# Kernel optimization log

Hardware: AMD Instinct MI355X
Metric: run time of the kernel (lower is better)

## Reference

```python
import jax, jax.numpy as jnp
import numpy as np

B, S, D, H = 8, 1024, 1024, 16
DH = D // H


def setup_inputs() -> dict:
    key = jax.random.key(0)
    ks = jax.random.split(key, 8)
    en = jax.random.normal(ks[0], (B, S, D), dtype=jnp.float32)
    fr = jax.random.normal(ks[1], (B, S, D), dtype=jnp.float32)
    l_en = jax.random.randint(ks[2], (B,), 1, S + 1)
    l_fr = jax.random.randint(ks[3], (B,), 1, S + 1)
    # nn.Linear-style params (weight stored [out, in])
    lim_q = 1.0 / np.sqrt(D)
    W_Q_w = jax.random.uniform(ks[4], (D, D), minval=-lim_q, maxval=lim_q, dtype=jnp.float32)
    W_Q_b = jax.random.uniform(ks[5], (D,), minval=-lim_q, maxval=lim_q, dtype=jnp.float32)
    W_KV_w = jax.random.uniform(ks[6], (2 * D, D), minval=-lim_q, maxval=lim_q, dtype=jnp.float32)
    W_KV_b = jax.random.uniform(ks[7], (2 * D,), minval=-lim_q, maxval=lim_q, dtype=jnp.float32)
    return {"en": en, "fr": fr, "l_en": l_en, "l_fr": l_fr,
            "W_Q_w": W_Q_w, "W_Q_b": W_Q_b, "W_KV_w": W_KV_w, "W_KV_b": W_KV_b}


def reference(en, fr, l_en, l_fr, W_Q_w, W_Q_b, W_KV_w, W_KV_b):
    # q from decoder (fr), k/v from encoder (en)
    q = (fr @ W_Q_w.T + W_Q_b).reshape(B, S, H, DH).transpose(0, 2, 1, 3)  # [B,H,S,DH]
    kv = (en @ W_KV_w.T + W_KV_b).reshape(B, S, 2, H, DH).transpose(2, 0, 3, 1, 4)
    k, v = kv[0], kv[1]  # [B,H,S,DH]

    # NOTE: original scales by sqrt(embedding_dim), not sqrt(head_dim)
    attn = jnp.einsum('bhqd,bhkd->bhqk', q, k) / jnp.sqrt(jnp.float32(D))

    pos = jnp.arange(S)
    mask_en = (pos[None, :] < l_en[:, None])  # [B,S] key mask
    mask_fr = (pos[None, :] < l_fr[:, None])  # [B,S] query mask
    mask = (mask_fr[:, :, None] & mask_en[:, None, :])[:, None, :, :]  # [B,1,Sq,Sk]

    attn = jnp.where(mask, attn, -jnp.inf)
    attn = jax.nn.softmax(attn, axis=-1)
    attn = jnp.nan_to_num(attn)  # fully-masked rows -> 0 (matches torch nan_to_num)

    out = jnp.einsum('bhqk,bhkd->bhqd', attn, v)  # [B,H,S,DH]
    return out.transpose(0, 2, 1, 3).reshape(B, S, D)
```

## Files before the change

### kernel.cpp

```cpp
#include <hip/hip_runtime.h>
#include <hip/hip_bf16.h>
#include <stdint.h>

typedef __bf16 bf16_t;
typedef bf16_t bf16x8 __attribute__((ext_vector_type(8)));
typedef float f32x4 __attribute__((ext_vector_type(4)));
typedef unsigned short ushortx8 __attribute__((ext_vector_type(8)));

__device__ __forceinline__ uint16_t f2bf(float f) {
  uint32_t u = __float_as_uint(f);
  uint32_t r = u + 0x7FFFu + ((u >> 16) & 1u);
  return (uint16_t)(r >> 16);
}

__device__ __forceinline__ int read_len(const int* __restrict__ p, int b) {
  bool is64 = (p[1] == 0) | (p[3] == 0) | (p[5] == 0) | (p[7] == 0);
  return is64 ? p[2 * b] : p[b];
}

#define GLDS16(gp, lp)                                                   \
  __builtin_amdgcn_global_load_lds(                                      \
      (const __attribute__((address_space(1))) uint32_t*)(gp),           \
      (__attribute__((address_space(3))) uint32_t*)(lp), 16, 0, 0)

__global__ void cvt4_kernel(const float* __restrict__ s0, uint16_t* __restrict__ d0, int n0,
                            const float* __restrict__ s1, uint16_t* __restrict__ d1, int n1,
                            const float* __restrict__ s2, uint16_t* __restrict__ d2, int n2,
                            const float* __restrict__ s3, uint16_t* __restrict__ d3, int n3,
                            const int* __restrict__ msk0, const int* __restrict__ msk1) {
  int e = (blockIdx.x * blockDim.x + threadIdx.x) * 8;
  const float* s;
  uint16_t* d;
  const int* msk = nullptr;
  if (e < n0) { s = s0 + e; d = d0 + e; msk = msk0; }
  else if ((e -= n0) < n1) { s = s1 + e; d = d1 + e; msk = msk1; }
  else if ((e -= n1) < n2) { s = s2 + e; d = d2 + e; }
  else if ((e -= n2) < n3) { s = s3 + e; d = d3 + e; }
  else return;
  if (msk) {
    int row = (e >> 10) & 1023, b = e >> 20;
    int need = (read_len(msk, b) + 127) & ~127;
    if (row >= need) return;
  }
  const float4 v0 = *reinterpret_cast<const float4*>(s);
  const float4 v1 = *reinterpret_cast<const float4*>(s + 4);
  ushortx8 o;
  o[0] = f2bf(v0.x); o[1] = f2bf(v0.y); o[2] = f2bf(v0.z); o[3] = f2bf(v0.w);
  o[4] = f2bf(v1.x); o[5] = f2bf(v1.y); o[6] = f2bf(v1.z); o[7] = f2bf(v1.w);
  *reinterpret_cast<ushortx8*>(d) = o;
}

__global__ __launch_bounds__(512) void gemm_fast(
    const uint16_t* __restrict__ frB, const uint16_t* __restrict__ enB,
    const uint16_t* __restrict__ wq, const uint16_t* __restrict__ wkv,
    const float* __restrict__ bq, const float* __restrict__ bkv,
    const int* __restrict__ l_en_p, const int* __restrict__ l_fr_p,
    uint16_t* __restrict__ Qb,
    uint16_t* __restrict__ Kb,
    uint16_t* __restrict__ Vb) {
  __shared__ __attribute__((aligned(16))) uint16_t As[3][128 * 64];
  __shared__ __attribute__((aligned(16))) uint16_t Bs[2][128 * 64];
  const int t = threadIdx.x;
  const int lane = t & 63;
  const int w = t >> 6;
  const int wm = w >> 2, wn = w & 3;
  const int l15 = lane & 15, lg = lane >> 4;

  const int orig = blockIdx.x;
  const int xcd = orig & 7;
  const int slot = orig >> 3;
  const bool isQ = slot < 64;
  int b, bn;
  if (isQ) { b = slot >> 3; bn = (slot & 7) * 128; }
  else { int s2 = slot - 64; b = s2 >> 4; bn = (s2 & 15) * 128; }
  const int i = (xcd - b) & 7;
  const int bm = b * 1024 + i * 128;

  const int need = isQ ? read_len(l_fr_p, b) : read_len(l_en_p, b);
  if (i * 128 >= need) return;

  const uint16_t* Bw = isQ ? wq : wkv;
  const float* bias = isQ ? bq : bkv;
  const float scale = isQ ? 0.03125f : 1.0f;
  const uint16_t* Ab = isQ ? frB : enB;

  f32x4 acc[4][2];
#pragma unroll
  for (int ii = 0; ii < 4; ++ii)
#pragma unroll
    for (int j = 0; j < 2; ++j) acc[ii][j] = (f32x4){0.f, 0.f, 0.f, 0.f};

  auto stageB = [&](int buf, int kt) {
#pragma unroll
    for (int ii = 0; ii < 2; ++ii) {
      int g = t + 512 * ii;
      int L = g ^ ((g >> 3) & 7);
      int row = L >> 3, k8 = L & 7;
      GLDS16(Bw + (size_t)(bn + row) * 1024 + kt + k8 * 8, &Bs[buf][g * 8]);
    }
  };
  auto stageA = [&](int buf, int kt) {
#pragma unroll
    for (int ii = 0; ii < 2; ++ii) {
      int g = t + 512 * ii;
      int L = g ^ ((g >> 3) & 7);
      int row = L >> 3, k8 = L & 7;
      GLDS16(Ab + (size_t)(bm + row) * 1024 + kt + k8 * 8, &As[buf][g * 8]);
    }
  };
  auto computeAB = [&](int bufA, int bufB) {
#pragma unroll
    for (int ks = 0; ks < 2; ++ks) {
      const int kb = ks * 64 + lg * 16;
      bf16x8 af[4], bf[2];
#pragma unroll
      for (int mf = 0; mf < 4; ++mf) {
        int row = wm * 64 + mf * 16 + l15;
        int byte = (row * 128 + kb) ^ ((row & 7) << 4);
        af[mf] = *reinterpret_cast<const bf16x8*>(
            reinterpret_cast<const char*>(As[bufA]) + byte);
      }
#pragma unroll
      for (int nf = 0; nf < 2; ++nf) {
        int row = wn * 32 + nf * 16 + l15;
        int byte = (row * 128 + kb) ^ ((row & 7) << 4);
        bf[nf] = *reinterpret_cast<const bf16x8*>(
            reinterpret_cast<const char*>(Bs[bufB]) + byte);
      }
#pragma unroll
      for (int mf = 0; mf < 4; ++mf)
#pragma unroll
        for (int nf = 0; nf < 2; ++nf)
          acc[mf][nf] = __builtin_amdgcn_mfma_f32_16x16x32_bf16(
              af[mf], bf[nf], acc[mf][nf], 0, 0, 0);
    }
  };

  stageA(0, 0);
  stageB(0, 0);
  stageA(1, 64);
  asm volatile("s_waitcnt vmcnt(2)" ::: "memory");
  __builtin_amdgcn_s_barrier();
  __builtin_amdgcn_sched_barrier(0);
  int aC = 0, bC = 0;
  for (int tt = 0; tt < 16; ++tt) {
    if (tt + 1 < 16) stageB(bC ^ 1, (tt + 1) * 64);
    if (tt + 2 < 16) stageA(aC >= 1 ? aC - 1 : aC + 2, (tt + 2) * 64);
    computeAB(aC, bC);
    if (tt < 15) {
      if (tt < 14) asm volatile("s_waitcnt vmcnt(2)" ::: "memory");
      else         asm volatile("s_waitcnt vmcnt(0)" ::: "memory");
      __builtin_amdgcn_s_barrier();
      __builtin_amdgcn_sched_barrier(0);
    }
    aC = (aC == 2) ? 0 : aC + 1;
    bC ^= 1;
  }

#pragma unroll
  for (int mf = 0; mf < 4; ++mf) {
#pragma unroll
    for (int nf = 0; nf < 2; ++nf) {
      int n = bn + wn * 32 + nf * 16 + l15;
      float bv = bias[n];
#pragma unroll
      for (int r = 0; r < 4; ++r) {
        int m = bm + wm * 64 + mf * 16 + lg * 4 + r;
        float v = (acc[mf][nf][r] + bv) * scale;
        uint16_t o = f2bf(v);
        int bb = m >> 10, s = m & 1023;
        if (isQ) {
          int h = n >> 6, d = n & 63;
          Qb[((((bb * 16 + h) << 10) | s) << 6) | d] = o;
        } else if (n < 1024) {
          int h = n >> 6, d = n & 63;
          Kb[((((bb * 16 + h) << 10) | s) << 6) | d] = o;
        } else {
          int n2 = n - 1024;
          int h = n2 >> 6, d = n2 & 63;
          Vb[((((bb * 16 + h) << 6) | d) << 10) | s] = o;
        }
      }
    }
  }
}

__global__ __launch_bounds__(256) void gemm_fb(
    const float* __restrict__ frF, const float* __restrict__ enF,
    const uint16_t* __restrict__ wq, const uint16_t* __restrict__ wkv,
    const float* __restrict__ bq, const float* __restrict__ bkv,
    const int* __restrict__ l_en_p, const int* __restrict__ l_fr_p,
    uint16_t* __restrict__ Qb, uint16_t* __restrict__ Kb,
    uint16_t* __restrict__ Vb) {
  __shared__ __attribute__((aligned(16))) uint16_t As[2][128 * 64];
  __shared__ __attribute__((aligned(16))) uint16_t Bs[2][128 * 64];
  const int t = threadIdx.x;
  const int lane = t & 63;
  const int w = t >> 6;
  const int wm = w >> 1, wn = w & 1;
  const int l15 = lane & 15, lg = lane >> 4;

  const int orig = blockIdx.x;
  const int xcd = orig & 7;
  const int slot = orig >> 3;
  const bool isQ = slot < 64;
  int b, bn;
  if (isQ) { b = slot >> 3; bn = (slot & 7) * 128; }
  else { int s2 = slot - 64; b = s2 >> 4; bn = (s2 & 15) * 128; }
  const int i = (xcd - b) & 7;
  const int bm = b * 1024 + i * 128;

  const int need = isQ ? read_len(l_fr_p, b) : read_len(l_en_p, b);
  if (i * 128 >= need) return;

  const uint16_t* Bw = isQ ? wq : wkv;
  const float* bias = isQ ? bq : bkv;
  const float scale = isQ ? 0.03125f : 1.0f;
  const float* Af = isQ ? frF : enF;

  f32x4 acc[4][4];
#pragma unroll
  for (int ii = 0; ii < 4; ++ii)
#pragma unroll
    for (int j = 0; j < 4; ++j) acc[ii][j] = (f32x4){0.f, 0.f, 0.f, 0.f};

  float4 ar0[4], ar1[4];

  auto stageB = [&](int buf, int kt) {
#pragma unroll
    for (int ii = 0; ii < 4; ++ii) {
      int g = t + 256 * ii;
      int L = g ^ ((g >> 3) & 7);
      int row = L >> 3, k8 = L & 7;
      GLDS16(Bw + (size_t)(bn + row) * 1024 + kt + k8 * 8, &Bs[buf][g * 8]);
    }
  };
  auto loadA_f32 = [&](int kt) {
#pragma unroll
    for (int ii = 0; ii < 4; ++ii) {
      int L = t + 256 * ii;
      int row = L >> 3, k8 = L & 7;
      const float* src = Af + (size_t)(bm + row) * 1024 + kt + k8 * 8;
      ar0[ii] = *reinterpret_cast<const float4*>(src);
      ar1[ii] = *reinterpret_cast<const float4*>(src + 4);
    }
  };
  auto writeA = [&](int buf) {
#pragma unroll
    for (int ii = 0; ii < 4; ++ii) {
      int L = t + 256 * ii;
      int row = L >> 3, k8 = L & 7;
      ushortx8 o;
      o[0] = f2bf(ar0[ii].x); o[1] = f2bf(ar0[ii].y);
      o[2] = f2bf(ar0[ii].z); o[3] = f2bf(ar0[ii].w);
      o[4] = f2bf(ar1[ii].x); o[5] = f2bf(ar1[ii].y);
      o[6] = f2bf(ar1[ii].z); o[7] = f2bf(ar1[ii].w);
      int byte = (row * 128 + k8 * 16) ^ ((row & 7) << 4);
      *reinterpret_cast<ushortx8*>(reinterpret_cast<char*>(As[buf]) + byte) = o;
    }
  };
  auto compute = [&](int buf) {
#pragma unroll
    for (int ks = 0; ks < 2; ++ks) {
      const int kb = ks * 64 + lg * 16;
      bf16x8 af[4], bf[4];
#pragma unroll
      for (int mf = 0; mf < 4; ++mf) {
        int row = wm * 64 + mf * 16 + l15;
        int byte = (row * 128 + kb) ^ ((row & 7) << 4);
        af[mf] = *reinterpret_cast<const bf16x8*>(
            reinterpret_cast<const char*>(As[buf]) + byte);
      }
#pragma unroll
      for (int nf = 0; nf < 4; ++nf) {
        int row = wn * 64 + nf * 16 + l15;
        int byte = (row * 128 + kb) ^ ((row & 7) << 4);
        bf[nf] = *reinterpret_cast<const bf16x8*>(
            reinterpret_cast<const char*>(Bs[buf]) + byte);
      }
#pragma unroll
      for (int mf = 0; mf < 4; ++mf)
#pragma unroll
        for (int nf = 0; nf < 4; ++nf)
          acc[mf][nf] = __builtin_amdgcn_mfma_f32_16x16x32_bf16(
              af[mf], bf[nf], acc[mf][nf], 0, 0, 0);
    }
  };
  loadA_f32(0);
  stageB(0, 0);
  writeA(0);
  __syncthreads();
#pragma unroll 2
  for (int tt = 0; tt < 16; ++tt) {
    const int cur = tt & 1;
    const int ktn = (tt + 1) * 64;
    if (tt < 15) { stageB(cur ^ 1, ktn); loadA_f32(ktn); }
    compute(cur);
    if (tt < 15) writeA(cur ^ 1);
    __syncthreads();
  }

#pragma unroll
  for (int mf = 0; mf < 4; ++mf) {
#pragma unroll
    for (int nf = 0; nf < 4; ++nf) {
      int n = bn + wn * 64 + nf * 16 + l15;
      float bv = bias[n];
#pragma unroll
      for (int r = 0; r < 4; ++r) {
        int m = bm + wm * 64 + mf * 16 + lg * 4 + r;
        float v = (acc[mf][nf][r] + bv) * scale;
        uint16_t o = f2bf(v);
        int bb = m >> 10, s = m & 1023;
        if (isQ) {
          int h = n >> 6, d = n & 63;
          Qb[((((bb * 16 + h) << 10) | s) << 6) | d] = o;
        } else if (n < 1024) {
          int h = n >> 6, d = n & 63;
          Kb[((((bb * 16 + h) << 10) | s) << 6) | d] = o;
        } else {
          int n2 = n - 1024;
          int h = n2 >> 6, d = n2 & 63;
          Vb[((((bb * 16 + h) << 6) | d) << 10) | s] = o;
        }
      }
    }
  }
}

__global__ __launch_bounds__(512) void attn_kernel(
    const uint16_t* __restrict__ Qb,
    const uint16_t* __restrict__ Kb,
    const uint16_t* __restrict__ Vt,
    const int* __restrict__ l_en_p, const int* __restrict__ l_fr_p,
    float* __restrict__ out) {
  __shared__ __attribute__((aligned(16))) uint16_t Ks[3][64 * 64];
  __shared__ __attribute__((aligned(16))) uint16_t Vs[3][64 * 64];
  __shared__ __attribute__((aligned(16))) bf16_t Ps[8][16][72];
  const int t = threadIdx.x;
  const int lane = t & 63, w = t >> 6;
  const int l15 = lane & 15, lg = lane >> 4;
  const int orig = blockIdx.x;
  const int xcd = orig & 7;
  const int slot = orig >> 3;
  const int b = slot >> 4;
  const int rest = slot & 15;
  const int h = xcd + 8 * (rest >> 3);
  const int q0 = (rest & 7) << 7;
  const int bh = b * 16 + h;
  const int len_en = read_len(l_en_p, b);
  const int len_fr = read_len(l_fr_p, b);

  if (q0 >= len_fr) {
    for (int i = t; i < 128 * 64; i += 512) {
      int rr = i >> 6, cc = i & 63;
      out[(size_t)(b * 1024 + q0 + rr) * 1024 + h * 64 + cc] = 0.f;
    }
    return;
  }

  const uint16_t* qbase =
      Qb + ((size_t)bh * 1024 + q0 + w * 16 + l15) * 64 + lg * 8;
  const bf16x8 aq0 = *reinterpret_cast<const bf16x8*>(qbase);
  const bf16x8 aq1 = *reinterpret_cast<const bf16x8*>(qbase + 32);

  float mrow[4], lrow[4];
  f32x4 oacc[4];
#pragma unroll
  for (int r = 0; r < 4; ++r) { mrow[r] = -1e30f; lrow[r] = 0.f; }
#pragma unroll
  for (int df = 0; df < 4; ++df) oacc[df] = (f32x4){0.f, 0.f, 0.f, 0.f};

  auto stage = [&](int buf, int j0) {
    int g = t;
    int L = g ^ ((g >> 3) & 7);
    int row = L >> 3, k8 = L & 7;
    GLDS16(Kb + ((size_t)bh * 1024 + j0 + row) * 64 + k8 * 8, &Ks[buf][g * 8]);
    GLDS16(Vt + ((size_t)bh * 64 + row) * 1024 + j0 + k8 * 8, &Vs[buf][g * 8]);
  };

  const int ntiles = (len_en + 63) >> 6;
  stage(0, 0);
  if (ntiles > 1) {
    stage(1, 64);
    asm volatile("s_waitcnt vmcnt(2)" ::: "memory");
  } else {
    asm volatile("s_waitcnt vmcnt(0)" ::: "memory");
  }
  __builtin_amdgcn_s_barrier();
  __builtin_amdgcn_sched_barrier(0);

  int cur = 0;
  for (int tt = 0; tt < ntiles; ++tt) {
    const int j0 = tt * 64;
    if (tt + 2 < ntiles) stage(cur >= 1 ? cur - 1 : 2, (tt + 2) * 64);

    f32x4 sc[4];
#pragma unroll
    for (int nf = 0; nf < 4; ++nf) sc[nf] = (f32x4){0.f, 0.f, 0.f, 0.f};
    __builtin_amdgcn_s_setprio(1);
#pragma unroll
    for (int ks = 0; ks < 2; ++ks) {
      const bf16x8 aq = ks ? aq1 : aq0;
      const int kb = ks * 64 + lg * 16;
#pragma unroll
      for (int nf = 0; nf < 4; ++nf) {
        int row = nf * 16 + l15;
        int byte = (row * 128 + kb) ^ ((row & 7) << 4);
        bf16x8 bk = *reinterpret_cast<const bf16x8*>(
            reinterpret_cast<const char*>(Ks[cur]) + byte);
        sc[nf] = __builtin_amdgcn_mfma_f32_16x16x32_bf16(aq, bk, sc[nf], 0, 0, 0);
      }
    }
    __builtin_amdgcn_s_setprio(0);
#pragma unroll
    for (int nf = 0; nf < 4; ++nf) {
      int col = j0 + nf * 16 + l15;
      if (col >= len_en) sc[nf] = (f32x4){-1e30f, -1e30f, -1e30f, -1e30f};
    }
    float tm[4];
#pragma unroll
    for (int r = 0; r < 4; ++r)
      tm[r] = fmaxf(fmaxf(sc[0][r], sc[1][r]), fmaxf(sc[2][r], sc[3][r]));
#pragma unroll
    for (int off = 1; off < 16; off <<= 1)
#pragma unroll
      for (int r = 0; r < 4; ++r) tm[r] = fmaxf(tm[r], __shfl_xor(tm[r], off));

    bool small = (tm[0] <= mrow[0] + 8.f) && (tm[1] <= mrow[1] + 8.f) &&
                 (tm[2] <= mrow[2] + 8.f) && (tm[3] <= mrow[3] + 8.f);
    if (!__all(small)) {
      float fac[4];
#pragma unroll
      for (int r = 0; r < 4; ++r) {
        float mn = fmaxf(mrow[r], tm[r]);
        fac[r] = __expf(mrow[r] - mn);
        mrow[r] = mn;
      }
#pragma unroll
      for (int r = 0; r < 4; ++r) lrow[r] *= fac[r];
#pragma unroll
      for (int df = 0; df < 4; ++df)
#pragma unroll
        for (int r = 0; r < 4; ++r) oacc[df][r] *= fac[r];
    }
    float ps[4] = {0.f, 0.f, 0.f, 0.f};
#pragma unroll
    for (int nf = 0; nf < 4; ++nf)
#pragma unroll
      for (int r = 0; r < 4; ++r) {
        float p = __expf(sc[nf][r] - mrow[r]);
        ps[r] += p;
        Ps[w][lg * 4 + r][nf * 16 + l15] = (bf16_t)p;
      }
#pragma unroll
    for (int off = 1; off < 16; off <<= 1)
#pragma unroll
      for (int r = 0; r < 4; ++r) ps[r] += __shfl_xor(ps[r], off);
#pragma unroll
    for (int r = 0; r < 4; ++r) lrow[r] += ps[r];

    __builtin_amdgcn_s_setprio(1);
#pragma unroll
    for (int ks = 0; ks < 2; ++ks) {
      const bf16x8 pa = *reinterpret_cast<const bf16x8*>(
          &Ps[w][l15][0] + ks * 32 + lg * 8);
#pragma unroll
      for (int df = 0; df < 4; ++df) {
        int row = df * 16 + l15;
        int byte = (row * 128 + ks * 64 + lg * 16) ^ ((row & 7) << 4);
        bf16x8 bv = *reinterpret_cast<const bf16x8*>(
            reinterpret_cast<const char*>(Vs[cur]) + byte);
        oacc[df] = __builtin_amdgcn_mfma_f32_16x16x32_bf16(pa, bv, oacc[df], 0, 0, 0);
      }
    }
    __builtin_amdgcn_s_setprio(0);

    if (tt + 1 < ntiles) {
      if (tt + 2 < ntiles) asm volatile("s_waitcnt vmcnt(2)" ::: "memory");
      else                 asm volatile("s_waitcnt vmcnt(0)" ::: "memory");
      __builtin_amdgcn_s_barrier();
      __builtin_amdgcn_sched_barrier(0);
    }
    cur = (cur == 2) ? 0 : cur + 1;
  }

#pragma unroll
  for (int df = 0; df < 4; ++df)
#pragma unroll
    for (int r = 0; r < 4; ++r) {
      int q = q0 + w * 16 + lg * 4 + r;
      float inv = (q < len_fr && lrow[r] > 0.f) ? 1.0f / lrow[r] : 0.f;
      out[(size_t)(b * 1024 + q) * 1024 + h * 64 + df * 16 + l15] =
          oacc[df][r] * inv;
    }
}

extern "C" void kernel_launch(void* const* d_in, const int* in_sizes, int n_in,
                              void* d_out, int out_size, void* d_ws,
                              size_t ws_size, hipStream_t stream) {
  const float* en = (const float*)d_in[0];
  const float* fr = (const float*)d_in[1];
  const int* l_en = (const int*)d_in[2];
  const int* l_fr = (const int*)d_in[3];
  const float* wq = (const float*)d_in[4];
  const float* bq = (const float*)d_in[5];
  const float* wkv = (const float*)d_in[6];
  const float* bkv = (const float*)d_in[7];
  float* out = (float*)d_out;

  char* ws = (char*)d_ws;
  uint16_t* wq_bf = (uint16_t*)(ws);
  uint16_t* wkv_bf = (uint16_t*)(ws + 2097152);
  uint16_t* Qbuf = (uint16_t*)(ws + 6291456);
  uint16_t* Kbuf = (uint16_t*)(ws + 23068672);
  uint16_t* Vtbuf = (uint16_t*)(ws + 39845888);
  uint16_t* fr_bf = (uint16_t*)(ws + 56623104);
  uint16_t* en_bf = (uint16_t*)(ws + 73400320);
  const bool pre = ws_size >= 90177536ull;

  if (pre) {
    cvt4_kernel<<<9728, 256, 0, stream>>>(fr, fr_bf, 8388608,
                                          en, en_bf, 8388608,
                                          wq, wq_bf, 1048576,
                                          wkv, wkv_bf, 2097152,
                                          l_fr, l_en);
    gemm_fast<<<1536, 512, 0, stream>>>(fr_bf, en_bf, wq_bf, wkv_bf, bq, bkv,
                                        l_en, l_fr, Qbuf, Kbuf, Vtbuf);
  } else {
    cvt4_kernel<<<1536, 256, 0, stream>>>(wq, wq_bf, 1048576,
                                          wkv, wkv_bf, 2097152,
                                          nullptr, nullptr, 0,
                                          nullptr, nullptr, 0,
                                          nullptr, nullptr);
    gemm_fb<<<1536, 256, 0, stream>>>(fr, en, wq_bf, wkv_bf, bq, bkv,
                                      l_en, l_fr, Qbuf, Kbuf, Vtbuf);
  }

  attn_kernel<<<1024, 512, 0, stream>>>(Qbuf, Kbuf, Vtbuf, l_en, l_fr, out);
}
```

Measured before the change: 108.2 us.

## Use persistent blocks with per-XCD atomic work counters in GEMM and attention

Converts gemm_fast and attn_kernel into persistent kernels launched with 512 blocks. Each block repeatedly pulls a slot index from a per-XCD global atomic counter, and the counters are reset at the start of the conversion kernel. The goal is to balance work when masked tiles exit early with uneven cost, and to avoid the launch and tail cost of many short blocks. In exchange it adds atomic and barrier overhead per work item, and it depends on the conversion kernel always running first to reset the counters.

```diff
diff --git a/kernel.cpp b/kernel.cpp
--- a/kernel.cpp
+++ b/kernel.cpp
@@ -6,6 +6,9 @@
 typedef bf16_t bf16x8 __attribute__((ext_vector_type(8)));
 typedef float f32x4 __attribute__((ext_vector_type(4)));
 typedef unsigned short ushortx8 __attribute__((ext_vector_type(8)));
+
+__device__ int g_qctr[8];
+__device__ int g_actr[8];
 
 __device__ __forceinline__ uint16_t f2bf(float f) {
   uint32_t u = __float_as_uint(f);
@@ -28,6 +31,10 @@
                             const float* __restrict__ s2, uint16_t* __restrict__ d2, int n2,
                             const float* __restrict__ s3, uint16_t* __restrict__ d3, int n3,
                             const int* __restrict__ msk0, const int* __restrict__ msk1) {
+  if (blockIdx.x == 0 && threadIdx.x < 16) {
+    if (threadIdx.x < 8) g_qctr[threadIdx.x] = 0;
+    else g_actr[threadIdx.x - 8] = 0;
+  }
   int e = (blockIdx.x * blockDim.x + threadIdx.x) * 8;
   const float* s;
   uint16_t* d;
@@ -60,10 +67,150 @@
     uint16_t* __restrict__ Vb) {
   __shared__ __attribute__((aligned(16))) uint16_t As[3][128 * 64];
   __shared__ __attribute__((aligned(16))) uint16_t Bs[2][128 * 64];
+  __shared__ int slot_sh;
   const int t = threadIdx.x;
   const int lane = t & 63;
   const int w = t >> 6;
   const int wm = w >> 2, wn = w & 3;
+  const int l15 = lane & 15, lg = lane >> 4;
+  const int xcd = blockIdx.x & 7;
+
+  for (;;) {
+    if (t == 0) slot_sh = atomicAdd(&g_qctr[xcd], 1);
+    __syncthreads();
+    const int slot = slot_sh;
+    __syncthreads();
+    if (slot >= 192) break;
+
+    const bool isQ = slot < 64;
+    int b, bn;
+    if (isQ) { b = slot >> 3; bn = (slot & 7) * 128; }
+    else { int s2 = slot - 64; b = s2 >> 4; bn = (s2 & 15) * 128; }
+    const int i = (xcd - b) & 7;
+    const int bm = b * 1024 + i * 128;
+    const int need = isQ ? read_len(l_fr_p, b) : read_len(l_en_p, b);
+    if (i * 128 >= need) continue;
+
+    const uint16_t* Bw = isQ ? wq : wkv;
+    const float* bias = isQ ? bq : bkv;
+    const float scale = isQ ? 0.03125f : 1.0f;
+    const uint16_t* Ab = isQ ? frB : enB;
+
+    f32x4 acc[4][2];
+#pragma unroll
+    for (int ii = 0; ii < 4; ++ii)
+#pragma unroll
+      for (int j = 0; j < 2; ++j) acc[ii][j] = (f32x4){0.f, 0.f, 0.f, 0.f};
+
+    auto stageB = [&](int buf, int kt) {
+#pragma unroll
+      for (int ii = 0; ii < 2; ++ii) {
+        int g = t + 512 * ii;
+        int L = g ^ ((g >> 3) & 7);
+        int row = L >> 3, k8 = L & 7;
+        GLDS16(Bw + (size_t)(bn + row) * 1024 + kt + k8 * 8, &Bs[buf][g * 8]);
+      }
+    };
+    auto stageA = [&](int buf, int kt) {
+#pragma unroll
+      for (int ii = 0; ii < 2; ++ii) {
+        int g = t + 512 * ii;
+        int L = g ^ ((g >> 3) & 7);
+        int row = L >> 3, k8 = L & 7;
+        GLDS16(Ab + (size_t)(bm + row) * 1024 + kt + k8 * 8, &As[buf][g * 8]);
+      }
+    };
+    auto computeAB = [&](int bufA, int bufB) {
+#pragma unroll
+      for (int ks = 0; ks < 2; ++ks) {
+        const int kb = ks * 64 + lg * 16;
+        bf16x8 af[4], bf[2];
+#pragma unroll
+        for (int mf = 0; mf < 4; ++mf) {
+          int row = wm * 64 + mf * 16 + l15;
+          int byte = (row * 128 + kb) ^ ((row & 7) << 4);
+          af[mf] = *reinterpret_cast<const bf16x8*>(
+              reinterpret_cast<const char*>(As[bufA]) + byte);
+        }
+#pragma unroll
+        for (int nf = 0; nf < 2; ++nf) {
+          int row = wn * 32 + nf * 16 + l15;
+          int byte = (row * 128 + kb) ^ ((row & 7) << 4);
+          bf[nf] = *reinterpret_cast<const bf16x8*>(
+              reinterpret_cast<const char*>(Bs[bufB]) + byte);
+        }
+#pragma unroll
+        for (int mf = 0; mf < 4; ++mf)
+#pragma unroll
+          for (int nf = 0; nf < 2; ++nf)
+            acc[mf][nf] = __builtin_amdgcn_mfma_f32_16x16x32_bf16(
+                af[mf], bf[nf], acc[mf][nf], 0, 0, 0);
+      }
+    };
+
+    stageA(0, 0);
+    stageB(0, 0);
+    stageA(1, 64);
+    asm volatile("s_waitcnt vmcnt(2)" ::: "memory");
+    __builtin_amdgcn_s_barrier();
+    __builtin_amdgcn_sched_barrier(0);
+    int aC = 0, bC = 0;
+    for (int tt = 0; tt < 16; ++tt) {
+      if (tt + 1 < 16) stageB(bC ^ 1, (tt + 1) * 64);
+      if (tt + 2 < 16) stageA(aC >= 1 ? aC - 1 : aC + 2, (tt + 2) * 64);
+      computeAB(aC, bC);
+      if (tt < 15) {
+        if (tt < 14) asm volatile("s_waitcnt vmcnt(2)" ::: "memory");
+        else         asm volatile("s_waitcnt vmcnt(0)" ::: "memory");
+        __builtin_amdgcn_s_barrier();
+        __builtin_amdgcn_sched_barrier(0);
+      }
+      aC = (aC == 2) ? 0 : aC + 1;
+      bC ^= 1;
+    }
+
+#pragma unroll
+    for (int mf = 0; mf < 4; ++mf) {
+#pragma unroll
+      for (int nf = 0; nf < 2; ++nf) {
+        int n = bn + wn * 32 + nf * 16 + l15;
+        float bv = bias[n];
+#pragma unroll
+        for (int r = 0; r < 4; ++r) {
+          int m = bm + wm * 64 + mf * 16 + lg * 4 + r;
+          float v = (acc[mf][nf][r] + bv) * scale;
+          uint16_t o = f2bf(v);
+          int bb = m >> 10, s = m & 1023;
+          if (isQ) {
+            int h = n >> 6, d = n & 63;
+            Qb[((((bb * 16 + h) << 10) | s) << 6) | d] = o;
+          } else if (n < 1024) {
+            int h = n >> 6, d = n & 63;
+            Kb[((((bb * 16 + h) << 10) | s) << 6) | d] = o;
+          } else {
+            int n2 = n - 1024;
+            int h = n2 >> 6, d = n2 & 63;
+            Vb[((((bb * 16 + h) << 6) | d) << 10) | s] = o;
+          }
+        }
+      }
+    }
+  }
+}
+
+__global__ __launch_bounds__(256) void gemm_fb(
+    const float* __restrict__ frF, const float* __restrict__ enF,
+    const uint16_t* __restrict__ wq, const uint16_t* __restrict__ wkv,
+    const float* __restrict__ bq, const float* __restrict__ bkv,
+    const int* __restrict__ l_en_p, const int* __restrict__ l_fr_p,
+    uint16_t* __restrict__ Qb, uint16_t* __restrict__ Kb,
+    uint16_t* __restrict__ Vb) {
+  __shared__ __attribute__((aligned(16))) uint16_t As[2][128 * 64];
+  __shared__ __attribute__((aligned(16))) uint16_t Bs[2][128 * 64];
+  const int t = threadIdx.x;
+  const int lane = t & 63;
+  const int w = t >> 6;
+  const int wm = w >> 1, wn = w & 1;
   const int l15 = lane & 15, lg = lane >> 4;
 
   const int orig = blockIdx.x;
@@ -82,86 +229,95 @@
   const uint16_t* Bw = isQ ? wq : wkv;
   const float* bias = isQ ? bq : bkv;
   const float scale = isQ ? 0.03125f : 1.0f;
-  const uint16_t* Ab = isQ ? frB : enB;
-
-  f32x4 acc[4][2];
+  const float* Af = isQ ? frF : enF;
+
+  f32x4 acc[4][4];
 #pragma unroll
   for (int ii = 0; ii < 4; ++ii)
 #pragma unroll
-    for (int j = 0; j < 2; ++j) acc[ii][j] = (f32x4){0.f, 0.f, 0.f, 0.f};
+    for (int j = 0; j < 4; ++j) acc[ii][j] = (f32x4){0.f, 0.f, 0.f, 0.f};
+
+  float4 ar0[4], ar1[4];
 
   auto stageB = [&](int buf, int kt) {
 #pragma unroll
-    for (int ii = 0; ii < 2; ++ii) {
-      int g = t + 512 * ii;
+    for (int ii = 0; ii < 4; ++ii) {
+      int g = t + 256 * ii;
       int L = g ^ ((g >> 3) & 7);
       int row = L >> 3, k8 = L & 7;
       GLDS16(Bw + (size_t)(bn + row) * 1024 + kt + k8 * 8, &Bs[buf][g * 8]);
     }
   };
-  auto stageA = [&](int buf, int kt) {
-#pragma unroll
-    for (int ii = 0; ii < 2; ++ii) {
-      int g = t + 512 * ii;
-      int L = g ^ ((g >> 3) & 7);
+  auto loadA_f32 = [&](int kt) {
+#pragma unroll
+    for (int ii = 0; ii < 4; ++ii) {
+      int L = t + 256 * ii;
       int row = L >> 3, k8 = L & 7;
-      GLDS16(Ab + (size_t)(bm + row) * 1024 + kt + k8 * 8, &As[buf][g * 8]);
+      const float* src = Af + (size_t)(bm + row) * 1024 + kt + k8 * 8;
+      ar0[ii] = *reinterpret_cast<const float4*>(src);
+      ar1[ii] = *reinterpret_cast<const float4*>(src + 4);
     }
   };
-  auto computeAB = [&](int bufA, int bufB) {
+  auto writeA = [&](int buf) {
+#pragma unroll
+    for (int ii = 0; ii < 4; ++ii) {
+      int L = t + 256 * ii;
+      int row = L >> 3, k8 = L & 7;
+      ushortx8 o;
+      o[0] = f2bf(ar0[ii].x); o[1] = f2bf(ar0[ii].y);
+      o[2] = f2bf(ar0[ii].z); o[3] = f2bf(ar0[ii].w);
+      o[4] = f2bf(ar1[ii].x); o[5] = f2bf(ar1[ii].y);
+      o[6] = f2bf(ar1[ii].z); o[7] = f2bf(ar1[ii].w);
+      int byte = (row * 128 + k8 * 16) ^ ((row & 7) << 4);
+      *reinterpret_cast<ushortx8*>(reinterpret_cast<char*>(As[buf]) + byte) = o;
+    }
+  };
+  auto compute = [&](int buf) {
 #pragma unroll
     for (int ks = 0; ks < 2; ++ks) {
       const int kb = ks * 64 + lg * 16;
-      bf16x8 af[4], bf[2];
+      bf16x8 af[4], bf[4];
 #pragma unroll
       for (int mf = 0; mf < 4; ++mf) {
         int row = wm * 64 + mf * 16 + l15;
         int byte = (row * 128 + kb) ^ ((row & 7) << 4);
         af[mf] = *reinterpret_cast<const bf16x8*>(
-            reinterpret_cast<const char*>(As[bufA]) + byte);
-      }
-#pragma unroll
-      for (int nf = 0; nf < 2; ++nf) {
-        int row = wn * 32 + nf * 16 + l15;
+            reinterpret_cast<const char*>(As[buf]) + byte);
+      }
+#pragma unroll
+      for (int nf = 0; nf < 4; ++nf) {
+        int row = wn * 64 + nf * 16 + l15;
         int byte = (row * 128 + kb) ^ ((row & 7) << 4);
         bf[nf] = *reinterpret_cast<const bf16x8*>(
-            reinterpret_cast<const char*>(Bs[bufB]) + byte);
+            reinterpret_cast<const char*>(Bs[buf]) + byte);
       }
 #pragma unroll
       for (int mf = 0; mf < 4; ++mf)
 #pragma unroll
-        for (int nf = 0; nf < 2; ++nf)
+        for (int nf = 0; nf < 4; ++nf)
           acc[mf][nf] = __builtin_amdgcn_mfma_f32_16x16x32_bf16(
               af[mf], bf[nf], acc[mf][nf], 0, 0, 0);
     }
   };
-
-  stageA(0, 0);
+  loadA_f32(0);
   stageB(0, 0);
-  stageA(1, 64);
-  asm volatile("s_waitcnt vmcnt(2)" ::: "memory");
-  __builtin_amdgcn_s_barrier();
-  __builtin_amdgcn_sched_barrier(0);
-  int aC = 0, bC = 0;
+  writeA(0);
+  __syncthreads();
+#pragma unroll 2
   for (int tt = 0; tt < 16; ++tt) {
-    if (tt + 1 < 16) stageB(bC ^ 1, (tt + 1) * 64);
-    if (tt + 2 < 16) stageA(aC >= 1 ? aC - 1 : aC + 2, (tt + 2) * 64);
-    computeAB(aC, bC);
-    if (tt < 15) {
-      if (tt < 14) asm volatile("s_waitcnt vmcnt(2)" ::: "memory");
-      else         asm volatile("s_waitcnt vmcnt(0)" ::: "memory");
-      __builtin_amdgcn_s_barrier();
-      __builtin_amdgcn_sched_barrier(0);
-    }
-    aC = (aC == 2) ? 0 : aC + 1;
-    bC ^= 1;
+    const int cur = tt & 1;
+    const int ktn = (tt + 1) * 64;
+    if (tt < 15) { stageB(cur ^ 1, ktn); loadA_f32(ktn); }
+    compute(cur);
+    if (tt < 15) writeA(cur ^ 1);
+    __syncthreads();
   }
 
 #pragma unroll
   for (int mf = 0; mf < 4; ++mf) {
 #pragma unroll
-    for (int nf = 0; nf < 2; ++nf) {
-      int n = bn + wn * 32 + nf * 16 + l15;
+    for (int nf = 0; nf < 4; ++nf) {
+      int n = bn + wn * 64 + nf * 16 + l15;
       float bv = bias[n];
 #pragma unroll
       for (int r = 0; r < 4; ++r) {
@@ -185,149 +341,6 @@
   }
 }
 
-__global__ __launch_bounds__(256) void gemm_fb(
-    const float* __restrict__ frF, const float* __restrict__ enF,
-    const uint16_t* __restrict__ wq, const uint16_t* __restrict__ wkv,
-    const float* __restrict__ bq, const float* __restrict__ bkv,
-    const int* __restrict__ l_en_p, const int* __restrict__ l_fr_p,
-    uint16_t* __restrict__ Qb, uint16_t* __restrict__ Kb,
-    uint16_t* __restrict__ Vb) {
-  __shared__ __attribute__((aligned(16))) uint16_t As[2][128 * 64];
-  __shared__ __attribute__((aligned(16))) uint16_t Bs[2][128 * 64];
-  const int t = threadIdx.x;
-  const int lane = t & 63;
-  const int w = t >> 6;
-  const int wm = w >> 1, wn = w & 1;
-  const int l15 = lane & 15, lg = lane >> 4;
-
-  const int orig = blockIdx.x;
-  const int xcd = orig & 7;
-  const int slot = orig >> 3;
-  const bool isQ = slot < 64;
-  int b, bn;
-  if (isQ) { b = slot >> 3; bn = (slot & 7) * 128; }
-  else { int s2 = slot - 64; b = s2 >> 4; bn = (s2 & 15) * 128; }
-  const int i = (xcd - b) & 7;
-  const int bm = b * 1024 + i * 128;
-
-  const int need = isQ ? read_len(l_fr_p, b) : read_len(l_en_p, b);
-  if (i * 128 >= need) return;
-
-  const uint16_t* Bw = isQ ? wq : wkv;
-  const float* bias = isQ ? bq : bkv;
-  const float scale = isQ ? 0.03125f : 1.0f;
-  const float* Af = isQ ? frF : enF;
-
-  f32x4 acc[4][4];
-#pragma unroll
-  for (int ii = 0; ii < 4; ++ii)
-#pragma unroll
-    for (int j = 0; j < 4; ++j) acc[ii][j] = (f32x4){0.f, 0.f, 0.f, 0.f};
-
-  float4 ar0[4], ar1[4];
-
-  auto stageB = [&](int buf, int kt) {
-#pragma unroll
-    for (int ii = 0; ii < 4; ++ii) {
-      int g = t + 256 * ii;
-      int L = g ^ ((g >> 3) & 7);
-      int row = L >> 3, k8 = L & 7;
-      GLDS16(Bw + (size_t)(bn + row) * 1024 + kt + k8 * 8, &Bs[buf][g * 8]);
-    }
-  };
-  auto loadA_f32 = [&](int kt) {
-#pragma unroll
-    for (int ii = 0; ii < 4; ++ii) {
-      int L = t + 256 * ii;
-      int row = L >> 3, k8 = L & 7;
-      const float* src = Af + (size_t)(bm + row) * 1024 + kt + k8 * 8;
-      ar0[ii] = *reinterpret_cast<const float4*>(src);
-      ar1[ii] = *reinterpret_cast<const float4*>(src + 4);
-    }
-  };
-  auto writeA = [&](int buf) {
-#pragma unroll
-    for (int ii = 0; ii < 4; ++ii) {
-      int L = t + 256 * ii;
-      int row = L >> 3, k8 = L & 7;
-      ushortx8 o;
-      o[0] = f2bf(ar0[ii].x); o[1] = f2bf(ar0[ii].y);
-      o[2] = f2bf(ar0[ii].z); o[3] = f2bf(ar0[ii].w);
-      o[4] = f2bf(ar1[ii].x); o[5] = f2bf(ar1[ii].y);
-      o[6] = f2bf(ar1[ii].z); o[7] = f2bf(ar1[ii].w);
-      int byte = (row * 128 + k8 * 16) ^ ((row & 7) << 4);
-      *reinterpret_cast<ushortx8*>(reinterpret_cast<char*>(As[buf]) + byte) = o;
-    }
-  };
-  auto compute = [&](int buf) {
-#pragma unroll
-    for (int ks = 0; ks < 2; ++ks) {
-      const int kb = ks * 64 + lg * 16;
-      bf16x8 af[4], bf[4];
-#pragma unroll
-      for (int mf = 0; mf < 4; ++mf) {
-        int row = wm * 64 + mf * 16 + l15;
-        int byte = (row * 128 + kb) ^ ((row & 7) << 4);
-        af[mf] = *reinterpret_cast<const bf16x8*>(
-            reinterpret_cast<const char*>(As[buf]) + byte);
-      }
-#pragma unroll
-      for (int nf = 0; nf < 4; ++nf) {
-        int row = wn * 64 + nf * 16 + l15;
-        int byte = (row * 128 + kb) ^ ((row & 7) << 4);
-        bf[nf] = *reinterpret_cast<const bf16x8*>(
-            reinterpret_cast<const char*>(Bs[buf]) + byte);
-      }
-#pragma unroll
-      for (int mf = 0; mf < 4; ++mf)
-#pragma unroll
-        for (int nf = 0; nf < 4; ++nf)
-          acc[mf][nf] = __builtin_amdgcn_mfma_f32_16x16x32_bf16(
-              af[mf], bf[nf], acc[mf][nf], 0, 0, 0);
-    }
-  };
-  loadA_f32(0);
-  stageB(0, 0);
-  writeA(0);
-  __syncthreads();
-#pragma unroll 2
-  for (int tt = 0; tt < 16; ++tt) {
-    const int cur = tt & 1;
-    const int ktn = (tt + 1) * 64;
-    if (tt < 15) { stageB(cur ^ 1, ktn); loadA_f32(ktn); }
-    compute(cur);
-    if (tt < 15) writeA(cur ^ 1);
-    __syncthreads();
-  }
-
-#pragma unroll
-  for (int mf = 0; mf < 4; ++mf) {
-#pragma unroll
-    for (int nf = 0; nf < 4; ++nf) {
-      int n = bn + wn * 64 + nf * 16 + l15;
-      float bv = bias[n];
-#pragma unroll
-      for (int r = 0; r < 4; ++r) {
-        int m = bm + wm * 64 + mf * 16 + lg * 4 + r;
-        float v = (acc[mf][nf][r] + bv) * scale;
-        uint16_t o = f2bf(v);
-        int bb = m >> 10, s = m & 1023;
-        if (isQ) {
-          int h = n >> 6, d = n & 63;
-          Qb[((((bb * 16 + h) << 10) | s) << 6) | d] = o;
-        } else if (n < 1024) {
-          int h = n >> 6, d = n & 63;
-          Kb[((((bb * 16 + h) << 10) | s) << 6) | d] = o;
-        } else {
-          int n2 = n - 1024;
-          int h = n2 >> 6, d = n2 & 63;
-          Vb[((((bb * 16 + h) << 6) | d) << 10) | s] = o;
-        }
-      }
-    }
-  }
-}
-
 __global__ __launch_bounds__(512) void attn_kernel(
     const uint16_t* __restrict__ Qb,
     const uint16_t* __restrict__ Kb,
@@ -337,163 +350,171 @@
   __shared__ __attribute__((aligned(16))) uint16_t Ks[3][64 * 64];
   __shared__ __attribute__((aligned(16))) uint16_t Vs[3][64 * 64];
   __shared__ __attribute__((aligned(16))) bf16_t Ps[8][16][72];
+  __shared__ int slot_sh;
   const int t = threadIdx.x;
   const int lane = t & 63, w = t >> 6;
   const int l15 = lane & 15, lg = lane >> 4;
-  const int orig = blockIdx.x;
-  const int xcd = orig & 7;
-  const int slot = orig >> 3;
-  const int b = slot >> 4;
-  const int rest = slot & 15;
-  const int h = xcd + 8 * (rest >> 3);
-  const int q0 = (rest & 7) << 7;
-  const int bh = b * 16 + h;
-  const int len_en = read_len(l_en_p, b);
-  const int len_fr = read_len(l_fr_p, b);
-
-  if (q0 >= len_fr) {
-    for (int i = t; i < 128 * 64; i += 512) {
-      int rr = i >> 6, cc = i & 63;
-      out[(size_t)(b * 1024 + q0 + rr) * 1024 + h * 64 + cc] = 0.f;
-    }
-    return;
-  }
-
-  const uint16_t* qbase =
-      Qb + ((size_t)bh * 1024 + q0 + w * 16 + l15) * 64 + lg * 8;
-  const bf16x8 aq0 = *reinterpret_cast<const bf16x8*>(qbase);
-  const bf16x8 aq1 = *reinterpret_cast<const bf16x8*>(qbase + 32);
-
-  float mrow[4], lrow[4];
-  f32x4 oacc[4];
-#pragma unroll
-  for (int r = 0; r < 4; ++r) { mrow[r] = -1e30f; lrow[r] = 0.f; }
-#pragma unroll
-  for (int df = 0; df < 4; ++df) oacc[df] = (f32x4){0.f, 0.f, 0.f, 0.f};
-
-  auto stage = [&](int buf, int j0) {
-    int g = t;
-    int L = g ^ ((g >> 3) & 7);
-    int row = L >> 3, k8 = L & 7;
-    GLDS16(Kb + ((size_t)bh * 1024 + j0 + row) * 64 + k8 * 8, &Ks[buf][g * 8]);
-    GLDS16(Vt + ((size_t)bh * 64 + row) * 1024 + j0 + k8 * 8, &Vs[buf][g * 8]);
-  };
-
-  const int ntiles = (len_en + 63) >> 6;
-  stage(0, 0);
-  if (ntiles > 1) {
-    stage(1, 64);
-    asm volatile("s_waitcnt vmcnt(2)" ::: "memory");
-  } else {
-    asm volatile("s_waitcnt vmcnt(0)" ::: "memory");
-  }
-  __builtin_amdgcn_s_barrier();
-  __builtin_amdgcn_sched_barrier(0);
-
-  int cur = 0;
-  for (int tt = 0; tt < ntiles; ++tt) {
-    const int j0 = tt * 64;
-    if (tt + 2 < ntiles) stage(cur >= 1 ? cur - 1 : 2, (tt + 2) * 64);
-
-    f32x4 sc[4];
-#pragma unroll
-    for (int nf = 0; nf < 4; ++nf) sc[nf] = (f32x4){0.f, 0.f, 0.f, 0.f};
-    __builtin_amdgcn_s_setprio(1);
-#pragma unroll
-    for (int ks = 0; ks < 2; ++ks) {
-      const bf16x8 aq = ks ? aq1 : aq0;
-      const int kb = ks * 64 + lg * 16;
+  const int xcd = blockIdx.x & 7;
+
+  for (;;) {
+    if (t == 0) slot_sh = atomicAdd(&g_actr[xcd], 1);
+    __syncthreads();
+    const int slot = slot_sh;
+    __syncthreads();
+    if (slot >= 128) break;
+
+    const int b = slot >> 4;
+    const int rest = slot & 15;
+    const int h = xcd + 8 * (rest >> 3);
+    const int q0 = (rest & 7) << 7;
+    const int bh = b * 16 + h;
+    const int len_en = read_len(l_en_p, b);
+    const int len_fr = read_len(l_fr_p, b);
+
+    if (q0 >= len_fr) {
+      for (int i = t; i < 128 * 64; i += 512) {
+        int rr = i >> 6, cc = i & 63;
+        out[(size_t)(b * 1024 + q0 + rr) * 1024 + h * 64 + cc] = 0.f;
+      }
+      continue;
+    }
+
+    const uint16_t* qbase =
+        Qb + ((size_t)bh * 1024 + q0 + w * 16 + l15) * 64 + lg * 8;
+    const bf16x8 aq0 = *reinterpret_cast<const bf16x8*>(qbase);
+    const bf16x8 aq1 = *reinterpret_cast<const bf16x8*>(qbase + 32);
+
+    float mrow[4], lrow[4];
+    f32x4 oacc[4];
+#pragma unroll
+    for (int r = 0; r < 4; ++r) { mrow[r] = -1e30f; lrow[r] = 0.f; }
+#pragma unroll
+    for (int df = 0; df < 4; ++df) oacc[df] = (f32x4){0.f, 0.f, 0.f, 0.f};
+
+    auto stage = [&](int buf, int j0) {
+      int g = t;
+      int L = g ^ ((g >> 3) & 7);
+      int row = L >> 3, k8 = L & 7;
+      GLDS16(Kb + ((size_t)bh * 1024 + j0 + row) * 64 + k8 * 8, &Ks[buf][g * 8]);
+      GLDS16(Vt + ((size_t)bh * 64 + row) * 1024 + j0 + k8 * 8, &Vs[buf][g * 8]);
+    };
+
+    const int ntiles = (len_en + 63) >> 6;
+    stage(0, 0);
+    if (ntiles > 1) {
+      stage(1, 64);
+      asm volatile("s_waitcnt vmcnt(2)" ::: "memory");
+    } else {
+      asm volatile("s_waitcnt vmcnt(0)" ::: "memory");
+    }
+    __builtin_amdgcn_s_barrier();
+    __builtin_amdgcn_sched_barrier(0);
+
+    int cur = 0;
+    for (int tt = 0; tt < ntiles; ++tt) {
+      const int j0 = tt * 64;
+      if (tt + 2 < ntiles) stage(cur >= 1 ? cur - 1 : 2, (tt + 2) * 64);
+
+      f32x4 sc[4];
+#pragma unroll
+      for (int nf = 0; nf < 4; ++nf) sc[nf] = (f32x4){0.f, 0.f, 0.f, 0.f};
+      __builtin_amdgcn_s_setprio(1);
+#pragma unroll
+      for (int ks = 0; ks < 2; ++ks) {
+        const bf16x8 aq = ks ? aq1 : aq0;
+        const int kb = ks * 64 + lg * 16;
+#pragma unroll
+        for (int nf = 0; nf < 4; ++nf) {
+          int row = nf * 16 + l15;
+          int byte = (row * 128 + kb) ^ ((row & 7) << 4);
+          bf16x8 bk = *reinterpret_cast<const bf16x8*>(
+              reinterpret_cast<const char*>(Ks[cur]) + byte);
+          sc[nf] = __builtin_amdgcn_mfma_f32_16x16x32_bf16(aq, bk, sc[nf], 0, 0, 0);
+        }
+      }
+      __builtin_amdgcn_s_setprio(0);
 #pragma unroll
       for (int nf = 0; nf < 4; ++nf) {
-        int row = nf * 16 + l15;
-        int byte = (row * 128 + kb) ^ ((row & 7) << 4);
-        bf16x8 bk = *reinterpret_cast<const bf16x8*>(
-            reinterpret_cast<const char*>(Ks[cur]) + byte);
-        sc[nf] = __builtin_amdgcn_mfma_f32_16x16x32_bf16(aq, bk, sc[nf], 0, 0, 0);
-      }
-    }
-    __builtin_amdgcn_s_setprio(0);
-#pragma unroll
-    for (int nf = 0; nf < 4; ++nf) {
-      int col = j0 + nf * 16 + l15;
-      if (col >= len_en) sc[nf] = (f32x4){-1e30f, -1e30f, -1e30f, -1e30f};
-    }
-    float tm[4];
-#pragma unroll
-    for (int r = 0; r < 4; ++r)
-      tm[r] = fmaxf(fmaxf(sc[0][r], sc[1][r]), fmaxf(sc[2][r], sc[3][r]));
-#pragma unroll
-    for (int off = 1; off < 16; off <<= 1)
-#pragma unroll
-      for (int r = 0; r < 4; ++r) tm[r] = fmaxf(tm[r], __shfl_xor(tm[r], off));
-
-    bool small = (tm[0] <= mrow[0] + 8.f) && (tm[1] <= mrow[1] + 8.f) &&
-                 (tm[2] <= mrow[2] + 8.f) && (tm[3] <= mrow[3] + 8.f);
-    if (!__all(small)) {
-      float fac[4];
+        int col = j0 + nf * 16 + l15;
+        if (col >= len_en) sc[nf] = (f32x4){-1e30f, -1e30f, -1e30f, -1e30f};
+      }
+      float tm[4];
+#pragma unroll
+      for (int r = 0; r < 4; ++r)
+        tm[r] = fmaxf(fmaxf(sc[0][r], sc[1][r]), fmaxf(sc[2][r], sc[3][r]));
+#pragma unroll
+      for (int off = 1; off < 16; off <<= 1)
+#pragma unroll
+        for (int r = 0; r < 4; ++r) tm[r] = fmaxf(tm[r], __shfl_xor(tm[r], off));
+
+      bool small = (tm[0] <= mrow[0] + 8.f) && (tm[1] <= mrow[1] + 8.f) &&
+                   (tm[2] <= mrow[2] + 8.f) && (tm[3] <= mrow[3] + 8.f);
+      if (!__all(small)) {
+        float fac[4];
+#pragma unroll
+        for (int r = 0; r < 4; ++r) {
+          float mn = fmaxf(mrow[r], tm[r]);
+          fac[r] = __expf(mrow[r] - mn);
+          mrow[r] = mn;
+        }
+#pragma unroll
+        for (int r = 0; r < 4; ++r) lrow[r] *= fac[r];
+#pragma unroll
+        for (int df = 0; df < 4; ++df)
+#pragma unroll
+          for (int r = 0; r < 4; ++r) oacc[df][r] *= fac[r];
+      }
+      float ps[4] = {0.f, 0.f, 0.f, 0.f};
+#pragma unroll
+      for (int nf = 0; nf < 4; ++nf)
+#pragma unroll
+        for (int r = 0; r < 4; ++r) {
+          float p = __expf(sc[nf][r] - mrow[r]);
+          ps[r] += p;
+          Ps[w][lg * 4 + r][nf * 16 + l15] = (bf16_t)p;
+        }
+#pragma unroll
+      for (int off = 1; off < 16; off <<= 1)
+#pragma unroll
+        for (int r = 0; r < 4; ++r) ps[r] += __shfl_xor(ps[r], off);
+#pragma unroll
+      for (int r = 0; r < 4; ++r) lrow[r] += ps[r];
+
+      __builtin_amdgcn_s_setprio(1);
+#pragma unroll
+      for (int ks = 0; ks < 2; ++ks) {
+        const bf16x8 pa = *reinterpret_cast<const bf16x8*>(
+            &Ps[w][l15][0] + ks * 32 + lg * 8);
+#pragma unroll
+        for (int df = 0; df < 4; ++df) {
+          int row = df * 16 + l15;
+          int byte = (row * 128 + ks * 64 + lg * 16) ^ ((row & 7) << 4);
+          bf16x8 bv = *reinterpret_cast<const bf16x8*>(
+              reinterpret_cast<const char*>(Vs[cur]) + byte);
+          oacc[df] = __builtin_amdgcn_mfma_f32_16x16x32_bf16(pa, bv, oacc[df], 0, 0, 0);
+        }
+      }
+      __builtin_amdgcn_s_setprio(0);
+
+      if (tt + 1 < ntiles) {
+        if (tt + 2 < ntiles) asm volatile("s_waitcnt vmcnt(2)" ::: "memory");
+        else                 asm volatile("s_waitcnt vmcnt(0)" ::: "memory");
+        __builtin_amdgcn_s_barrier();
+        __builtin_amdgcn_sched_barrier(0);
+      }
+      cur = (cur == 2) ? 0 : cur + 1;
+    }
+
+#pragma unroll
+    for (int df = 0; df < 4; ++df)
 #pragma unroll
       for (int r = 0; r < 4; ++r) {
-        float mn = fmaxf(mrow[r], tm[r]);
-        fac[r] = __expf(mrow[r] - mn);
-        mrow[r] = mn;
-      }
-#pragma unroll
-      for (int r = 0; r < 4; ++r) lrow[r] *= fac[r];
-#pragma unroll
-      for (int df = 0; df < 4; ++df)
-#pragma unroll
-        for (int r = 0; r < 4; ++r) oacc[df][r] *= fac[r];
-    }
-    float ps[4] = {0.f, 0.f, 0.f, 0.f};
-#pragma unroll
-    for (int nf = 0; nf < 4; ++nf)
-#pragma unroll
-      for (int r = 0; r < 4; ++r) {
-        float p = __expf(sc[nf][r] - mrow[r]);
-        ps[r] += p;
-        Ps[w][lg * 4 + r][nf * 16 + l15] = (bf16_t)p;
-      }
-#pragma unroll
-    for (int off = 1; off < 16; off <<= 1)
-#pragma unroll
-      for (int r = 0; r < 4; ++r) ps[r] += __shfl_xor(ps[r], off);
-#pragma unroll
-    for (int r = 0; r < 4; ++r) lrow[r] += ps[r];
-
-    __builtin_amdgcn_s_setprio(1);
-#pragma unroll
-    for (int ks = 0; ks < 2; ++ks) {
-      const bf16x8 pa = *reinterpret_cast<const bf16x8*>(
-          &Ps[w][l15][0] + ks * 32 + lg * 8);
-#pragma unroll
-      for (int df = 0; df < 4; ++df) {
-        int row = df * 16 + l15;
-        int byte = (row * 128 + ks * 64 + lg * 16) ^ ((row & 7) << 4);
-        bf16x8 bv = *reinterpret_cast<const bf16x8*>(
-            reinterpret_cast<const char*>(Vs[cur]) + byte);
-        oacc[df] = __builtin_amdgcn_mfma_f32_16x16x32_bf16(pa, bv, oacc[df], 0, 0, 0);
-      }
-    }
-    __builtin_amdgcn_s_setprio(0);
-
-    if (tt + 1 < ntiles) {
-      if (tt + 2 < ntiles) asm volatile("s_waitcnt vmcnt(2)" ::: "memory");
-      else                 asm volatile("s_waitcnt vmcnt(0)" ::: "memory");
-      __builtin_amdgcn_s_barrier();
-      __builtin_amdgcn_sched_barrier(0);
-    }
-    cur = (cur == 2) ? 0 : cur + 1;
-  }
-
-#pragma unroll
-  for (int df = 0; df < 4; ++df)
-#pragma unroll
-    for (int r = 0; r < 4; ++r) {
-      int q = q0 + w * 16 + lg * 4 + r;
-      float inv = (q < len_fr && lrow[r] > 0.f) ? 1.0f / lrow[r] : 0.f;
-      out[(size_t)(b * 1024 + q) * 1024 + h * 64 + df * 16 + l15] =
-          oacc[df][r] * inv;
-    }
+        int q = q0 + w * 16 + lg * 4 + r;
+        float inv = (q < len_fr && lrow[r] > 0.f) ? 1.0f / lrow[r] : 0.f;
+        out[(size_t)(b * 1024 + q) * 1024 + h * 64 + df * 16 + l15] =
+            oacc[df][r] * inv;
+      }
+  }
 }
 
 extern "C" void kernel_launch(void* const* d_in, const int* in_sizes, int n_in,
@@ -525,8 +546,8 @@
                                           wq, wq_bf, 1048576,
                                           wkv, wkv_bf, 2097152,
                                           l_fr, l_en);
-    gemm_fast<<<1536, 512, 0, stream>>>(fr_bf, en_bf, wq_bf, wkv_bf, bq, bkv,
-                                        l_en, l_fr, Qbuf, Kbuf, Vtbuf);
+    gemm_fast<<<512, 512, 0, stream>>>(fr_bf, en_bf, wq_bf, wkv_bf, bq, bkv,
+                                       l_en, l_fr, Qbuf, Kbuf, Vtbuf);
   } else {
     cvt4_kernel<<<1536, 256, 0, stream>>>(wq, wq_bf, 1048576,
                                           wkv, wkv_bf, 2097152,
@@ -537,5 +558,5 @@
                                       l_en, l_fr, Qbuf, Kbuf, Vtbuf);
   }
 
-  attn_kernel<<<1024, 512, 0, stream>>>(Qbuf, Kbuf, Vtbuf, l_en, l_fr, out);
-}
+  attn_kernel<<<512, 512, 0, stream>>>(Qbuf, Kbuf, Vtbuf, l_en, l_fr, out);
+}
```

New measurement: 138.0 us. 1.28x slower.
